# Optimization experiments

Measured on AMD Instinct MI355X. Metric: run time of the kernel, lower is better.

## Reference

```python
import jax, jax.numpy as jnp
import numpy as np

HIDDEN = 2048
NUM_HEADS = 16
NUM_KV_HEADS = 8
HEAD_DIM = 128
EPS = 1e-6
ROPE_THETA = 10000.0
SEQ = 2048
Q_SIZE = NUM_HEADS * HEAD_DIM
KV_SIZE = NUM_KV_HEADS * HEAD_DIM


def rmsnorm_f32(x, w, eps=EPS):
    # RMSNormF32: normalize in float32, scale by weight
    xf = x.astype(jnp.float32)
    var = jnp.mean(xf * xf, axis=-1, keepdims=True)
    return xf * jax.lax.rsqrt(var + eps) * w.astype(jnp.float32)


def apply_rope(x, cos, sin):
    # x: [S, H, D]; cos/sin: [S, D//2] (neox-style half split)
    half = x.shape[-1] // 2
    x1, x2 = x[..., :half], x[..., half:]
    c = cos[:, None, :]
    s = sin[:, None, :]
    return jnp.concatenate([x1 * c - x2 * s, x2 * c + x1 * s], axis=-1)


def setup_inputs() -> dict:
    key = jax.random.key(0)
    ks = jax.random.split(key, 6)
    return {
        "positions": jnp.arange(SEQ, dtype=jnp.int32),
        "hidden_states": jax.random.normal(ks[0], (SEQ, HIDDEN), jnp.float32),
        "ln_weight": 1.0 + 0.1 * jax.random.normal(ks[1], (HIDDEN,), jnp.float32),
        "qkv_weight": 0.02 * jax.random.normal(ks[2], (Q_SIZE + 2 * KV_SIZE, HIDDEN), jnp.float32),
        "q_norm_weight": 1.0 + 0.1 * jax.random.normal(ks[3], (HEAD_DIM,), jnp.float32),
        "k_norm_weight": 1.0 + 0.1 * jax.random.normal(ks[4], (HEAD_DIM,), jnp.float32),
        "o_weight": 0.02 * jax.random.normal(ks[5], (HIDDEN, Q_SIZE), jnp.float32),
    }


def reference(positions, hidden_states, ln_weight, qkv_weight, q_norm_weight, k_norm_weight, o_weight):
    S = hidden_states.shape[0]
    # 1. input RMSNorm (f32)
    normalized = rmsnorm_f32(hidden_states, ln_weight)
    # 2. fused QKV projection (no bias)
    qkv = normalized @ qkv_weight.T  # [S, q_size + 2*kv_size]
    q = qkv[:, :Q_SIZE].reshape(S, NUM_HEADS, HEAD_DIM)
    k = qkv[:, Q_SIZE:Q_SIZE + KV_SIZE].reshape(S, NUM_KV_HEADS, HEAD_DIM)
    v = qkv[:, Q_SIZE + KV_SIZE:].reshape(S, NUM_KV_HEADS, HEAD_DIM)
    # 3. RoPE (neox half-split, cache built from theta)
    inv_freq = ROPE_THETA ** (-jnp.arange(0, HEAD_DIM, 2, dtype=jnp.float32) / HEAD_DIM)
    freqs = positions.astype(jnp.float32)[:, None] * inv_freq[None, :]  # [S, D/2]
    cos, sin = jnp.cos(freqs), jnp.sin(freqs)
    q = apply_rope(q, cos, sin)
    k = apply_rope(k, cos, sin)
    # 4. per-head q/k RMSNorm (applied after RoPE, as in source)
    q = rmsnorm_f32(q, q_norm_weight)
    k = rmsnorm_f32(k, k_norm_weight)
    # 5. GQA expand kv heads
    rep = NUM_HEADS // NUM_KV_HEADS
    k = jnp.repeat(k, rep, axis=1)  # [S, NH, D]
    v = jnp.repeat(v, rep, axis=1)
    # 6. naive causal attention
    scores = jnp.einsum('shd,thd->hst', q, k) / (HEAD_DIM ** 0.5)  # [NH, S, S]
    causal = jnp.triu(jnp.ones((S, S), dtype=bool), k=1)
    scores = jnp.where(causal[None, :, :], -jnp.inf, scores)
    attn = jax.nn.softmax(scores, axis=-1)
    attn = jnp.nan_to_num(attn, nan=0.0)
    out = jnp.einsum('hst,thd->shd', attn, v).reshape(S, Q_SIZE)
    # 7. output projection
    return out @ o_weight.T
```

## Files before the change

### kernel.cpp

```cpp
#include <hip/hip_runtime.h>
#include <hip/hip_bf16.h>
#include <stdint.h>

typedef unsigned short u16;
typedef __attribute__((ext_vector_type(4))) float f32x4;
typedef __attribute__((ext_vector_type(8))) __bf16 bf16x8;
typedef __attribute__((ext_vector_type(8))) unsigned short u16x8;
typedef __attribute__((ext_vector_type(4))) unsigned short u16x4;

#define SEQ 2048
#define HID 2048
#define HD  128

__device__ __forceinline__ float b2f(u16 v) {
    union { float f; unsigned u; } c; c.u = ((unsigned)v) << 16; return c.f;
}
__device__ __forceinline__ u16 f2b(float f) {
    union { float f; unsigned u; } c; c.f = f;
    unsigned r = c.u + 0x7fffu + ((c.u >> 16) & 1u);
    return (u16)(r >> 16);
}
__device__ __forceinline__ bf16x8 tob(u16x8 v) {
    union { u16x8 u; bf16x8 b; } c; c.u = v; return c.b;
}
__device__ __forceinline__ u16x8 ld8(const u16* p) { return *(const u16x8*)p; }

typedef const __attribute__((address_space(1))) unsigned int* gas_ptr;
typedef __attribute__((address_space(3))) unsigned int* las_ptr;
__device__ __forceinline__ void gld16(const void* g, void* l) {
    __builtin_amdgcn_global_load_lds((gas_ptr)g, (las_ptr)l, 16, 0, 0);
}

__global__ __launch_bounds__(256) void k_conv(const float* __restrict__ src,
                                              u16* __restrict__ dst) {
    const size_t i = ((size_t)blockIdx.x * 256 + threadIdx.x) * 8;
    f32x4 a = *(const f32x4*)(src + i);
    f32x4 b = *(const f32x4*)(src + i + 4);
    u16x8 o;
#pragma unroll
    for (int e = 0; e < 4; ++e) { o[e] = f2b(a[e]); o[e + 4] = f2b(b[e]); }
    *(u16x8*)(dst + i) = o;
}

__global__ __launch_bounds__(256) void k_rmsnorm(const float* __restrict__ x,
                                                 const float* __restrict__ w,
                                                 u16* __restrict__ o) {
    const int row = blockIdx.x, t = threadIdx.x;
    const float* xr = x + (size_t)row * HID + t * 8;
    f32x4 xa = *(const f32x4*)xr;
    f32x4 xb = *(const f32x4*)(xr + 4);
    float xf[8]; float ss = 0.f;
#pragma unroll
    for (int e = 0; e < 4; ++e) { xf[e] = xa[e]; xf[e + 4] = xb[e]; }
#pragma unroll
    for (int e = 0; e < 8; ++e) ss += xf[e] * xf[e];
#pragma unroll
    for (int m = 32; m; m >>= 1) ss += __shfl_xor(ss, m);
    __shared__ float red[4];
    if ((t & 63) == 0) red[t >> 6] = ss;
    __syncthreads();
    ss = red[0] + red[1] + red[2] + red[3];
    const float sc = rsqrtf(ss * (1.0f / HID) + 1e-6f);
    f32x4 wa = *(const f32x4*)(w + t * 8);
    f32x4 wb = *(const f32x4*)(w + t * 8 + 4);
    u16x8 ov;
#pragma unroll
    for (int e = 0; e < 4; ++e) {
        ov[e] = f2b(xf[e] * sc * wa[e]);
        ov[e + 4] = f2b(xf[e + 4] * sc * wb[e]);
    }
    *(u16x8*)(o + (size_t)row * HID + t * 8) = ov;
}

#define STAGE_G(buf, k0)                                                      \
    do {                                                                      \
        char* a0 = (char*)&As[buf][0][0] + wave * 1024;                       \
        char* a1 = (char*)&As[buf][1][0] + wave * 1024;                       \
        char* b0 = (char*)&Bs[buf][0][0] + wave * 1024;                       \
        char* b1 = (char*)&Bs[buf][1][0] + wave * 1024;                       \
        gld16(ga + (k0), a0);                                                 \
        gld16(ga + (k0) + rowskip, a0 + 4096);                                \
        gld16(ga + (k0) + 32, a1);                                            \
        gld16(ga + (k0) + 32 + rowskip, a1 + 4096);                           \
        gld16(gb + (k0), b0);                                                 \
        gld16(gb + (k0) + rowskip, b0 + 4096);                                \
        gld16(gb + (k0) + 32, b1);                                            \
        gld16(gb + (k0) + 32 + rowskip, b1 + 4096);                           \
    } while (0)

__global__ __launch_bounds__(256) void k_gemm_qkv(const u16* __restrict__ A,
                                                  const u16* __restrict__ B,
                                                  u16* __restrict__ qraw,
                                                  u16* __restrict__ kraw,
                                                  u16* __restrict__ vtr,
                                                  int K) {
    __shared__ u16 As[2][2][128 * 32];
    __shared__ u16 Bs[2][2][128 * 32];
    const int tid = threadIdx.x;
    const int wave = tid >> 6, lane = tid & 63, quad = lane >> 4, l16 = lane & 15;
    const int wm = wave >> 1, wn = wave & 1;
    const int sw = (l16 >> 1) & 3;
    const int m0 = blockIdx.x * 128, n0 = blockIdx.y * 128;
    f32x4 acc[4][4];
#pragma unroll
    for (int i = 0; i < 4; ++i)
#pragma unroll
        for (int j = 0; j < 4; ++j) acc[i][j] = (f32x4){0.f, 0.f, 0.f, 0.f};

    const int gchunk = (tid & 3) ^ ((tid >> 3) & 3);
    const u16* ga = A + (size_t)(m0 + (tid >> 2)) * K + gchunk * 8;
    const u16* gb = B + (size_t)(n0 + (tid >> 2)) * K + gchunk * 8;
    const size_t rowskip = (size_t)64 * K;

    STAGE_G(0, 0);
    const int nk = K >> 6;
    for (int t = 0; t < nk; ++t) {
        const int cur = t & 1;
        if (t + 1 < nk) {
            STAGE_G(cur ^ 1, (t + 1) * 64);
            asm volatile("s_waitcnt vmcnt(8)" ::: "memory");
        } else {
            asm volatile("s_waitcnt vmcnt(0)" ::: "memory");
        }
        __builtin_amdgcn_s_barrier();
        asm volatile("" ::: "memory");
#pragma unroll
        for (int h = 0; h < 2; ++h) {
            const u16* as = &As[cur][h][0];
            const u16* bs = &Bs[cur][h][0];
            bf16x8 af[4], bfr[4];
#pragma unroll
            for (int i = 0; i < 4; ++i)
                af[i] = tob(ld8(as + (wm * 64 + i * 16 + l16) * 32 + ((quad ^ sw) << 3)));
#pragma unroll
            for (int j = 0; j < 4; ++j)
                bfr[j] = tob(ld8(bs + (wn * 64 + j * 16 + l16) * 32 + ((quad ^ sw) << 3)));
#pragma unroll
            for (int i = 0; i < 4; ++i)
#pragma unroll
                for (int j = 0; j < 4; ++j)
                    acc[i][j] = __builtin_amdgcn_mfma_f32_16x16x32_bf16(af[i], bfr[j], acc[i][j], 0, 0, 0);
        }
        asm volatile("" ::: "memory");
        __builtin_amdgcn_s_barrier();
    }
#pragma unroll
    for (int i = 0; i < 4; ++i) {
        const int row = m0 + wm * 64 + i * 16 + quad * 4;
#pragma unroll
        for (int j = 0; j < 4; ++j) {
            const int col = n0 + wn * 64 + j * 16 + l16;
#pragma unroll
            for (int r = 0; r < 4; ++r) {
                const u16 val = f2b(acc[i][j][r]);
                const int s = row + r;
                if (col < 2048) {
                    const int head = col >> 7, d = col & 127;
                    qraw[((size_t)head * SEQ + s) * HD + d] = val;
                } else if (col < 3072) {
                    const int c = col - 2048, kv = c >> 7, d = c & 127;
                    kraw[((size_t)kv * SEQ + s) * HD + d] = val;
                } else {
                    const int c = col - 3072, kv = c >> 7, d = c & 127;
                    vtr[(size_t)kv * HD * SEQ + (size_t)d * SEQ + s] = val;
                }
            }
        }
    }
}

__global__ __launch_bounds__(256) void k_gemm_of(const u16* __restrict__ A,
                                                 const u16* __restrict__ B,
                                                 float* __restrict__ C,
                                                 int N, int K) {
    __shared__ u16 As[2][2][128 * 32];
    __shared__ u16 Bs[2][2][128 * 32];
    const int tid = threadIdx.x;
    const int wave = tid >> 6, lane = tid & 63, quad = lane >> 4, l16 = lane & 15;
    const int wm = wave >> 1, wn = wave & 1;
    const int sw = (l16 >> 1) & 3;
    const int m0 = blockIdx.x * 128, n0 = blockIdx.y * 128;
    f32x4 acc[4][4];
#pragma unroll
    for (int i = 0; i < 4; ++i)
#pragma unroll
        for (int j = 0; j < 4; ++j) acc[i][j] = (f32x4){0.f, 0.f, 0.f, 0.f};

    const int gchunk = (tid & 3) ^ ((tid >> 3) & 3);
    const u16* ga = A + (size_t)(m0 + (tid >> 2)) * K + gchunk * 8;
    const u16* gb = B + (size_t)(n0 + (tid >> 2)) * K + gchunk * 8;
    const size_t rowskip = (size_t)64 * K;

    STAGE_G(0, 0);
    const int nk = K >> 6;
    for (int t = 0; t < nk; ++t) {
        const int cur = t & 1;
        if (t + 1 < nk) {
            STAGE_G(cur ^ 1, (t + 1) * 64);
            asm volatile("s_waitcnt vmcnt(8)" ::: "memory");
        } else {
            asm volatile("s_waitcnt vmcnt(0)" ::: "memory");
        }
        __builtin_amdgcn_s_barrier();
        asm volatile("" ::: "memory");
#pragma unroll
        for (int h = 0; h < 2; ++h) {
            const u16* as = &As[cur][h][0];
            const u16* bs = &Bs[cur][h][0];
            bf16x8 af[4], bfr[4];
#pragma unroll
            for (int i = 0; i < 4; ++i)
                af[i] = tob(ld8(as + (wm * 64 + i * 16 + l16) * 32 + ((quad ^ sw) << 3)));
#pragma unroll
            for (int j = 0; j < 4; ++j)
                bfr[j] = tob(ld8(bs + (wn * 64 + j * 16 + l16) * 32 + ((quad ^ sw) << 3)));
#pragma unroll
            for (int i = 0; i < 4; ++i)
#pragma unroll
                for (int j = 0; j < 4; ++j)
                    acc[i][j] = __builtin_amdgcn_mfma_f32_16x16x32_bf16(af[i], bfr[j], acc[i][j], 0, 0, 0);
        }
        asm volatile("" ::: "memory");
        __builtin_amdgcn_s_barrier();
    }
#pragma unroll
    for (int i = 0; i < 4; ++i) {
        const int row = m0 + wm * 64 + i * 16 + quad * 4;
#pragma unroll
        for (int j = 0; j < 4; ++j) {
            const int col = n0 + wn * 64 + j * 16 + l16;
#pragma unroll
            for (int r = 0; r < 4; ++r)
                C[(size_t)(row + r) * N + col] = acc[i][j][r];
        }
    }
}

__global__ __launch_bounds__(256) void k_ropenorm(const int* __restrict__ pos,
                                                  const float* __restrict__ qw,
                                                  const float* __restrict__ kw,
                                                  u16* __restrict__ qraw,
                                                  u16* __restrict__ kraw) {
    const int s = blockIdx.x;
    const int h = blockIdx.y * 4 + (threadIdx.x >> 6);
    const int d = threadIdx.x & 63;
    const bool isq = h < 16;
    u16* row = isq ? (qraw + ((size_t)h * SEQ + s) * HD)
                   : (kraw + ((size_t)(h - 16) * SEQ + s) * HD);
    const float x1 = b2f(row[d]), x2 = b2f(row[d + 64]);
    const float p = (float)pos[s];
    const float inv = exp2f(-(float)d * (2.0f / 128.0f) * 13.287712379549449f);
    const float fr = p * inv;
    const float c = cosf(fr), sn = sinf(fr);
    const float o1 = x1 * c - x2 * sn;
    const float o2 = x2 * c + x1 * sn;
    float ss = o1 * o1 + o2 * o2;
#pragma unroll
    for (int m = 32; m; m >>= 1) ss += __shfl_xor(ss, m);
    const float sc = rsqrtf(ss * (1.0f / HD) + 1e-6f);
    const float* w = isq ? qw : kw;
    row[d] = f2b(o1 * sc * w[d]);
    row[d + 64] = f2b(o2 * sc * w[d + 64]);
}

__global__ __launch_bounds__(256, 4) void k_attn(const u16* __restrict__ qh,
                                                 const u16* __restrict__ kh,
                                                 const u16* __restrict__ vt,
                                                 u16* __restrict__ out,
                                                 u16* __restrict__ po,
                                                 float* __restrict__ pl) {
    const int tid = threadIdx.x;
    const int wave = tid >> 6, lane = tid & 63, quad = lane >> 4, l16 = lane & 15;
    const int head = blockIdx.y;
    const int b = blockIdx.x;
    int qt, part, np;
    if (b < 11)      { qt = b;                      part = 0;            np = 1; }
    else if (b < 33) { qt = 11 + ((b - 11) >> 1);   part = (b - 11) & 1; np = 2; }
    else             { qt = 22 + (b - 33) / 3;      part = (b - 33) % 3; np = 3; }
    const int kvh = head >> 1;
    const int q0 = qt * 64;
    const int ntiles = qt + 1;

    __shared__ u16 Ks[64 * 128];
    __shared__ u16 Vts[128 * 64];
    __shared__ u16 Ps[4][16 * 64];

    const u16* qbase = qh + ((size_t)head * SEQ + q0 + wave * 16) * HD;
    bf16x8 aq[4];
#pragma unroll
    for (int kk = 0; kk < 4; ++kk)
        aq[kk] = tob(ld8(qbase + l16 * HD + kk * 32 + quad * 8));

    f32x4 acco[8];
#pragma unroll
    for (int j = 0; j < 8; ++j) acco[j] = (f32x4){0.f, 0.f, 0.f, 0.f};
    float lsum = 0.f;

    const float sc = 0.08838834764831845f;
    const u16* kbase = kh + (size_t)kvh * SEQ * HD;
    const u16* vbase = vt + (size_t)kvh * HD * SEQ;
    u16* pw = &Ps[wave][0];
    const int qrow_g = q0 + wave * 16 + l16;

    const u16* kg0 = kbase + (size_t)tid * 8;
    const u16* vg0 = vbase + (size_t)(tid >> 3) * SEQ + (size_t)(tid & 7) * 8;
    int kst[4], vst[4];
#pragma unroll
    for (int r = 0; r < 4; ++r) {
        const int krow = r * 16 + (tid >> 4);
        kst[r] = krow * 128 + (((tid & 15) ^ (krow & 7)) << 3);
        const int vrow = r * 32 + (tid >> 3);
        vst[r] = vrow * 64 + (((tid & 7) ^ (vrow & 7)) << 3);
    }

    u16x8 kreg[4], vreg[4];
    {
        const size_t koff = (size_t)part * 64;
#pragma unroll
        for (int r = 0; r < 4; ++r) {
            kreg[r] = ld8(kg0 + koff * HD + (size_t)r * 2048);
            vreg[r] = ld8(vg0 + koff + (size_t)r * 32 * SEQ);
        }
#pragma unroll
        for (int r = 0; r < 4; ++r) {
            *(u16x8*)(&Ks[0] + kst[r]) = kreg[r];
            *(u16x8*)(&Vts[0] + vst[r]) = vreg[r];
        }
    }
    __syncthreads();

    for (int kt = part; kt < ntiles; kt += np) {
        const bool havenext = (kt + np) < ntiles;
        if (havenext) {
            const size_t koff = (size_t)(kt + np) * 64;
#pragma unroll
            for (int r = 0; r < 4; ++r) {
                kreg[r] = ld8(kg0 + koff * HD + (size_t)r * 2048);
                vreg[r] = ld8(vg0 + koff + (size_t)r * 32 * SEQ);
            }
        }

        f32x4 accs[4];
#pragma unroll
        for (int j = 0; j < 4; ++j) accs[j] = (f32x4){0.f, 0.f, 0.f, 0.f};
#pragma unroll
        for (int kk = 0; kk < 4; ++kk) {
#pragma unroll
            for (int j = 0; j < 4; ++j) {
                const int krow = j * 16 + l16;
                const bf16x8 bk = tob(ld8(&Ks[0] + krow * 128 + (((kk * 4 + quad) ^ (krow & 7)) << 3)));
                accs[j] = __builtin_amdgcn_mfma_f32_16x16x32_bf16(bk, aq[kk], accs[j], 0, 0, 0);
            }
        }

        const int k0 = kt * 64;
#pragma unroll
        for (int j = 0; j < 4; ++j) {
            u16x4 pk;
#pragma unroll
            for (int r = 0; r < 4; ++r) {
                const int kpos = k0 + j * 16 + quad * 4 + r;
                const float pv = (kpos > qrow_g) ? 0.f : __expf(accs[j][r] * sc);
                lsum += pv;
                pk[r] = f2b(pv);
            }
            const int blk = (j * 2 + (quad >> 1)) ^ (l16 & 7);
            *(u16x4*)(pw + l16 * 64 + (blk << 3) + ((quad & 1) << 2)) = pk;
        }

#pragma unroll
        for (int kk = 0; kk < 2; ++kk) {
            const bf16x8 ap = tob(ld8(pw + l16 * 64 + (((kk * 4 + quad) ^ (l16 & 7)) << 3)));
#pragma unroll
            for (int j = 0; j < 8; ++j) {
                const int vrow = j * 16 + l16;
                const bf16x8 bv = tob(ld8(&Vts[0] + vrow * 64 + (((kk * 4 + quad) ^ (vrow & 7)) << 3)));
                acco[j] = __builtin_amdgcn_mfma_f32_16x16x32_bf16(ap, bv, acco[j], 0, 0, 0);
            }
        }

        __syncthreads();
        if (havenext) {
#pragma unroll
            for (int r = 0; r < 4; ++r) {
                *(u16x8*)(&Ks[0] + kst[r]) = kreg[r];
                *(u16x8*)(&Vts[0] + vst[r]) = vreg[r];
            }
        }
        __syncthreads();
    }

    float v = lsum;
    v += __shfl_xor(v, 16);
    v += __shfl_xor(v, 32);
    const int rowb = q0 + wave * 16 + quad * 4;

    if (np == 1) {
        f32x4 il;
#pragma unroll
        for (int r = 0; r < 4; ++r) il[r] = 1.0f / __shfl(v, quad * 4 + r);
#pragma unroll
        for (int j = 0; j < 8; ++j) {
            const int col = head * HD + j * 16 + l16;
#pragma unroll
            for (int r = 0; r < 4; ++r)
                out[(size_t)(rowb + r) * 2048 + col] = f2b(acco[j][r] * il[r]);
        }
    } else {
        u16* pob = po + (size_t)part * SEQ * 2048;
        float* plb = pl + (size_t)part * 16 * SEQ;
        if (lane < 16) plb[head * SEQ + q0 + wave * 16 + l16] = v;
#pragma unroll
        for (int j = 0; j < 8; ++j) {
            const int col = head * HD + j * 16 + l16;
#pragma unroll
            for (int r = 0; r < 4; ++r)
                pob[(size_t)(rowb + r) * 2048 + col] = f2b(acco[j][r]);
        }
    }
}

__global__ __launch_bounds__(256) void k_amerge(const u16* __restrict__ po,
                                                const float* __restrict__ pl,
                                                u16* __restrict__ out) {
    const int s = blockIdx.x + 704;
    const int qt = s >> 6;
    const int np = (qt > 21) ? 3 : 2;
    const int t = threadIdx.x;
    const int head = t >> 4;

    float l = 0.f;
#pragma unroll
    for (int p = 0; p < 3; ++p)
        if (p < np) l += pl[(size_t)p * 16 * SEQ + head * SEQ + s];
    const float il = 1.0f / l;

    float o[8] = {0.f, 0.f, 0.f, 0.f, 0.f, 0.f, 0.f, 0.f};
#pragma unroll
    for (int p = 0; p < 3; ++p) {
        if (p < np) {
            const u16x8 vv = ld8(po + (size_t)p * SEQ * 2048 + (size_t)s * 2048 + t * 8);
#pragma unroll
            for (int e = 0; e < 8; ++e) o[e] += b2f(vv[e]);
        }
    }
    u16x8 ov;
#pragma unroll
    for (int e = 0; e < 8; ++e) ov[e] = f2b(o[e] * il);
    *(u16x8*)(out + (size_t)s * 2048 + t * 8) = ov;
}

extern "C" void kernel_launch(void* const* d_in, const int* in_sizes, int n_in,
                              void* d_out, int out_size, void* d_ws, size_t ws_size,
                              hipStream_t stream) {
    const int*   positions = (const int*)d_in[0];
    const float* hidden   = (const float*)d_in[1];
    const float* lnw      = (const float*)d_in[2];
    const float* qkvw     = (const float*)d_in[3];
    const float* qnw      = (const float*)d_in[4];
    const float* knw      = (const float*)d_in[5];
    const float* ow       = (const float*)d_in[6];
    float* outp = (float*)d_out;

    char* ws = (char*)d_ws;
    const size_t MB = 1024ull * 1024ull;
    u16* normed = (u16*)(ws + 0 * MB);
    u16* qraw   = (u16*)(ws + 8 * MB);
    u16* kraw   = (u16*)(ws + 16 * MB);
    u16* vtr    = (u16*)(ws + 20 * MB);
    u16* qkvwb  = (u16*)(ws + 24 * MB);
    u16* owb    = (u16*)(ws + 0 * MB);
    u16* attno  = (u16*)(ws + 24 * MB);
    u16* po     = (u16*)(ws + 32 * MB);
    float* pl   = (float*)(ws + 56 * MB);

    k_rmsnorm <<<SEQ, 256, 0, stream>>>(hidden, lnw, normed);
    k_conv    <<<4096, 256, 0, stream>>>(qkvw, qkvwb);
    k_gemm_qkv<<<dim3(16, 32), 256, 0, stream>>>(normed, qkvwb, qraw, kraw, vtr, HID);
    k_ropenorm<<<dim3(SEQ, 6), 256, 0, stream>>>(positions, qnw, knw, qraw, kraw);
    k_conv    <<<2048, 256, 0, stream>>>(ow, owb);
    k_attn    <<<dim3(63, 16), 256, 0, stream>>>(qraw, kraw, vtr, attno, po, pl);
    k_amerge  <<<1344, 256, 0, stream>>>(po, pl, attno);
    k_gemm_of <<<dim3(16, 16), 256, 0, stream>>>(attno, owb, outp, HID, HID);
}
```

Before: 254.3 us.

## Deepen GEMM pipeline to four half-tile stages and fuse rmsnorm with weight conversion

Both GEMM kernels move from a double-buffered 64-wide K step to a four-slot ring of 32-wide K half-tiles, keeping three loads in flight with graded vmcnt waits. MFMA issue is also raised in priority with s_setprio. Separately, the input RMSNorm and the qkv weight fp32-to-bf16 conversion are merged into one launch to save a kernel launch. The deeper pipeline adds a barrier pair per 32-wide step instead of per 64-wide step, so there is more synchronisation, while shared memory use stays the same.

```diff
diff --git a/kernel.cpp b/kernel.cpp
--- a/kernel.cpp
+++ b/kernel.cpp
@@ -29,6 +29,49 @@
 typedef __attribute__((address_space(3))) unsigned int* las_ptr;
 __device__ __forceinline__ void gld16(const void* g, void* l) {
     __builtin_amdgcn_global_load_lds((gas_ptr)g, (las_ptr)l, 16, 0, 0);
+}
+
+__global__ __launch_bounds__(256) void k_prep(const float* __restrict__ x,
+                                              const float* __restrict__ w,
+                                              u16* __restrict__ normed,
+                                              const float* __restrict__ qkvw,
+                                              u16* __restrict__ qkvwb) {
+    const int b = blockIdx.x, t = threadIdx.x;
+    if (b < 2048) {
+        const int row = b;
+        const float* xr = x + (size_t)row * HID + t * 8;
+        f32x4 xa = *(const f32x4*)xr;
+        f32x4 xb = *(const f32x4*)(xr + 4);
+        float xf[8]; float ss = 0.f;
+#pragma unroll
+        for (int e = 0; e < 4; ++e) { xf[e] = xa[e]; xf[e + 4] = xb[e]; }
+#pragma unroll
+        for (int e = 0; e < 8; ++e) ss += xf[e] * xf[e];
+#pragma unroll
+        for (int m = 32; m; m >>= 1) ss += __shfl_xor(ss, m);
+        __shared__ float red[4];
+        if ((t & 63) == 0) red[t >> 6] = ss;
+        __syncthreads();
+        ss = red[0] + red[1] + red[2] + red[3];
+        const float sc = rsqrtf(ss * (1.0f / HID) + 1e-6f);
+        f32x4 wa = *(const f32x4*)(w + t * 8);
+        f32x4 wb = *(const f32x4*)(w + t * 8 + 4);
+        u16x8 ov;
+#pragma unroll
+        for (int e = 0; e < 4; ++e) {
+            ov[e] = f2b(xf[e] * sc * wa[e]);
+            ov[e + 4] = f2b(xf[e + 4] * sc * wb[e]);
+        }
+        *(u16x8*)(normed + (size_t)row * HID + t * 8) = ov;
+    } else {
+        const size_t i = ((size_t)(b - 2048) * 256 + t) * 8;
+        f32x4 a = *(const f32x4*)(qkvw + i);
+        f32x4 bb = *(const f32x4*)(qkvw + i + 4);
+        u16x8 o;
+#pragma unroll
+        for (int e = 0; e < 4; ++e) { o[e] = f2b(a[e]); o[e + 4] = f2b(bb[e]); }
+        *(u16x8*)(qkvwb + i) = o;
+    }
 }
 
 __global__ __launch_bounds__(256) void k_conv(const float* __restrict__ src,
@@ -42,51 +85,47 @@
     *(u16x8*)(dst + i) = o;
 }
 
-__global__ __launch_bounds__(256) void k_rmsnorm(const float* __restrict__ x,
-                                                 const float* __restrict__ w,
-                                                 u16* __restrict__ o) {
-    const int row = blockIdx.x, t = threadIdx.x;
-    const float* xr = x + (size_t)row * HID + t * 8;
-    f32x4 xa = *(const f32x4*)xr;
-    f32x4 xb = *(const f32x4*)(xr + 4);
-    float xf[8]; float ss = 0.f;
-#pragma unroll
-    for (int e = 0; e < 4; ++e) { xf[e] = xa[e]; xf[e + 4] = xb[e]; }
-#pragma unroll
-    for (int e = 0; e < 8; ++e) ss += xf[e] * xf[e];
-#pragma unroll
-    for (int m = 32; m; m >>= 1) ss += __shfl_xor(ss, m);
-    __shared__ float red[4];
-    if ((t & 63) == 0) red[t >> 6] = ss;
-    __syncthreads();
-    ss = red[0] + red[1] + red[2] + red[3];
-    const float sc = rsqrtf(ss * (1.0f / HID) + 1e-6f);
-    f32x4 wa = *(const f32x4*)(w + t * 8);
-    f32x4 wb = *(const f32x4*)(w + t * 8 + 4);
-    u16x8 ov;
-#pragma unroll
-    for (int e = 0; e < 4; ++e) {
-        ov[e] = f2b(xf[e] * sc * wa[e]);
-        ov[e + 4] = f2b(xf[e + 4] * sc * wb[e]);
-    }
-    *(u16x8*)(o + (size_t)row * HID + t * 8) = ov;
-}
-
-#define STAGE_G(buf, k0)                                                      \
+#define STAGE_H(buf, ht)                                                      \
     do {                                                                      \
-        char* a0 = (char*)&As[buf][0][0] + wave * 1024;                       \
-        char* a1 = (char*)&As[buf][1][0] + wave * 1024;                       \
-        char* b0 = (char*)&Bs[buf][0][0] + wave * 1024;                       \
-        char* b1 = (char*)&Bs[buf][1][0] + wave * 1024;                       \
-        gld16(ga + (k0), a0);                                                 \
-        gld16(ga + (k0) + rowskip, a0 + 4096);                                \
-        gld16(ga + (k0) + 32, a1);                                            \
-        gld16(ga + (k0) + 32 + rowskip, a1 + 4096);                           \
-        gld16(gb + (k0), b0);                                                 \
-        gld16(gb + (k0) + rowskip, b0 + 4096);                                \
-        gld16(gb + (k0) + 32, b1);                                            \
-        gld16(gb + (k0) + 32 + rowskip, b1 + 4096);                           \
+        char* ap = (char*)&As[buf][0] + wave * 1024;                          \
+        char* bp = (char*)&Bs[buf][0] + wave * 1024;                          \
+        const u16* gA = ga + (size_t)(ht) * 32;                               \
+        const u16* gB = gb + (size_t)(ht) * 32;                               \
+        gld16(gA, ap);                                                        \
+        gld16(gA + rowskip, ap + 4096);                                       \
+        gld16(gB, bp);                                                        \
+        gld16(gB + rowskip, bp + 4096);                                       \
     } while (0)
+
+#define GEMM_PIPE(K)                                                          \
+    STAGE_H(0, 0); STAGE_H(1, 1); STAGE_H(2, 2);                              \
+    const int NH = (K) >> 5;                                                  \
+    for (int ht = 0; ht < NH; ++ht) {                                         \
+        if (ht <= NH - 3)      asm volatile("s_waitcnt vmcnt(8)" ::: "memory");\
+        else if (ht == NH - 2) asm volatile("s_waitcnt vmcnt(4)" ::: "memory");\
+        else                   asm volatile("s_waitcnt vmcnt(0)" ::: "memory");\
+        __builtin_amdgcn_s_barrier();                                         \
+        asm volatile("" ::: "memory");                                        \
+        const u16* as = &As[ht & 3][0];                                       \
+        const u16* bs = &Bs[ht & 3][0];                                       \
+        bf16x8 af[4], bfr[4];                                                 \
+        _Pragma("unroll")                                                     \
+        for (int i = 0; i < 4; ++i)                                           \
+            af[i] = tob(ld8(as + (wm * 64 + i * 16 + l16) * 32 + ((quad ^ sw) << 3))); \
+        _Pragma("unroll")                                                     \
+        for (int j = 0; j < 4; ++j)                                           \
+            bfr[j] = tob(ld8(bs + (wn * 64 + j * 16 + l16) * 32 + ((quad ^ sw) << 3))); \
+        __builtin_amdgcn_s_setprio(1);                                        \
+        _Pragma("unroll")                                                     \
+        for (int i = 0; i < 4; ++i)                                           \
+            _Pragma("unroll")                                                 \
+            for (int j = 0; j < 4; ++j)                                       \
+                acc[i][j] = __builtin_amdgcn_mfma_f32_16x16x32_bf16(af[i], bfr[j], acc[i][j], 0, 0, 0); \
+        __builtin_amdgcn_s_setprio(0);                                        \
+        asm volatile("" ::: "memory");                                        \
+        __builtin_amdgcn_s_barrier();                                         \
+        if (ht + 3 < NH) { STAGE_H((ht + 3) & 3, ht + 3); }                   \
+    }
 
 __global__ __launch_bounds__(256) void k_gemm_qkv(const u16* __restrict__ A,
                                                   const u16* __restrict__ B,
@@ -94,8 +133,8 @@
                                                   u16* __restrict__ kraw,
                                                   u16* __restrict__ vtr,
                                                   int K) {
-    __shared__ u16 As[2][2][128 * 32];
-    __shared__ u16 Bs[2][2][128 * 32];
+    __shared__ u16 As[4][128 * 32];
+    __shared__ u16 Bs[4][128 * 32];
     const int tid = threadIdx.x;
     const int wave = tid >> 6, lane = tid & 63, quad = lane >> 4, l16 = lane & 15;
     const int wm = wave >> 1, wn = wave & 1;
@@ -112,38 +151,8 @@
     const u16* gb = B + (size_t)(n0 + (tid >> 2)) * K + gchunk * 8;
     const size_t rowskip = (size_t)64 * K;
 
-    STAGE_G(0, 0);
-    const int nk = K >> 6;
-    for (int t = 0; t < nk; ++t) {
-        const int cur = t & 1;
-        if (t + 1 < nk) {
-            STAGE_G(cur ^ 1, (t + 1) * 64);
-            asm volatile("s_waitcnt vmcnt(8)" ::: "memory");
-        } else {
-            asm volatile("s_waitcnt vmcnt(0)" ::: "memory");
-        }
-        __builtin_amdgcn_s_barrier();
-        asm volatile("" ::: "memory");
-#pragma unroll
-        for (int h = 0; h < 2; ++h) {
-            const u16* as = &As[cur][h][0];
-            const u16* bs = &Bs[cur][h][0];
-            bf16x8 af[4], bfr[4];
-#pragma unroll
-            for (int i = 0; i < 4; ++i)
-                af[i] = tob(ld8(as + (wm * 64 + i * 16 + l16) * 32 + ((quad ^ sw) << 3)));
-#pragma unroll
-            for (int j = 0; j < 4; ++j)
-                bfr[j] = tob(ld8(bs + (wn * 64 + j * 16 + l16) * 32 + ((quad ^ sw) << 3)));
-#pragma unroll
-            for (int i = 0; i < 4; ++i)
-#pragma unroll
-                for (int j = 0; j < 4; ++j)
-                    acc[i][j] = __builtin_amdgcn_mfma_f32_16x16x32_bf16(af[i], bfr[j], acc[i][j], 0, 0, 0);
-        }
-        asm volatile("" ::: "memory");
-        __builtin_amdgcn_s_barrier();
-    }
+    GEMM_PIPE(K)
+
 #pragma unroll
     for (int i = 0; i < 4; ++i) {
         const int row = m0 + wm * 64 + i * 16 + quad * 4;
@@ -173,8 +182,8 @@
                                                  const u16* __restrict__ B,
                                                  float* __restrict__ C,
                                                  int N, int K) {
-    __shared__ u16 As[2][2][128 * 32];
-    __shared__ u16 Bs[2][2][128 * 32];
+    __shared__ u16 As[4][128 * 32];
+    __shared__ u16 Bs[4][128 * 32];
     const int tid = threadIdx.x;
     const int wave = tid >> 6, lane = tid & 63, quad = lane >> 4, l16 = lane & 15;
     const int wm = wave >> 1, wn = wave & 1;
@@ -191,38 +200,8 @@
     const u16* gb = B + (size_t)(n0 + (tid >> 2)) * K + gchunk * 8;
     const size_t rowskip = (size_t)64 * K;
 
-    STAGE_G(0, 0);
-    const int nk = K >> 6;
-    for (int t = 0; t < nk; ++t) {
-        const int cur = t & 1;
-        if (t + 1 < nk) {
-            STAGE_G(cur ^ 1, (t + 1) * 64);
-            asm volatile("s_waitcnt vmcnt(8)" ::: "memory");
-        } else {
-            asm volatile("s_waitcnt vmcnt(0)" ::: "memory");
-        }
-        __builtin_amdgcn_s_barrier();
-        asm volatile("" ::: "memory");
-#pragma unroll
-        for (int h = 0; h < 2; ++h) {
-            const u16* as = &As[cur][h][0];
-            const u16* bs = &Bs[cur][h][0];
-            bf16x8 af[4], bfr[4];
-#pragma unroll
-            for (int i = 0; i < 4; ++i)
-                af[i] = tob(ld8(as + (wm * 64 + i * 16 + l16) * 32 + ((quad ^ sw) << 3)));
-#pragma unroll
-            for (int j = 0; j < 4; ++j)
-                bfr[j] = tob(ld8(bs + (wn * 64 + j * 16 + l16) * 32 + ((quad ^ sw) << 3)));
-#pragma unroll
-            for (int i = 0; i < 4; ++i)
-#pragma unroll
-                for (int j = 0; j < 4; ++j)
-                    acc[i][j] = __builtin_amdgcn_mfma_f32_16x16x32_bf16(af[i], bfr[j], acc[i][j], 0, 0, 0);
-        }
-        asm volatile("" ::: "memory");
-        __builtin_amdgcn_s_barrier();
-    }
+    GEMM_PIPE(K)
+
 #pragma unroll
     for (int i = 0; i < 4; ++i) {
         const int row = m0 + wm * 64 + i * 16 + quad * 4;
@@ -474,8 +453,7 @@
     u16* po     = (u16*)(ws + 32 * MB);
     float* pl   = (float*)(ws + 56 * MB);
 
-    k_rmsnorm <<<SEQ, 256, 0, stream>>>(hidden, lnw, normed);
-    k_conv    <<<4096, 256, 0, stream>>>(qkvw, qkvwb);
+    k_prep    <<<6144, 256, 0, stream>>>(hidden, lnw, normed, qkvw, qkvwb);
     k_gemm_qkv<<<dim3(16, 32), 256, 0, stream>>>(normed, qkvwb, qraw, kraw, vtr, HID);
     k_ropenorm<<<dim3(SEQ, 6), 256, 0, stream>>>(positions, qnw, knw, qraw, kraw);
     k_conv    <<<2048, 256, 0, stream>>>(ow, owb);
```

After: 263.0 us. 3.4% more time.
